# Performance work log

Measured on AMD Instinct MI355X. Metric: run time of the kernel, lower is better.

Reference implementation:

```python
import jax, jax.numpy as jnp
import numpy as np

HIDDEN = 4096
N_HEADS = 32
N_KV = 8
HEAD_DIM = 128
ROPE_THETA = 10000.0
B, S = 2, 2048


def _rope_neox(x, cos, sin):
    # x: [B,S,H,D]; cos/sin: [B,S,1,D/2]
    half = x.shape[-1] // 2
    x1, x2 = x[..., :half], x[..., half:]
    return jnp.concatenate([x1 * cos - x2 * sin, x2 * cos + x1 * sin], axis=-1)


def setup_inputs() -> dict:
    key = jax.random.key(0)
    k1, k2, k3 = jax.random.split(key, 3)
    hidden_states = jax.random.normal(k1, (B, S, HIDDEN), dtype=jnp.float32)
    positions = jnp.arange(B * S, dtype=jnp.int32).reshape(B, S)
    q_size = N_HEADS * HEAD_DIM
    kv_size = N_KV * HEAD_DIM
    w_qkv = jax.random.normal(k2, (HIDDEN, q_size + 2 * kv_size), dtype=jnp.float32) * (HIDDEN ** -0.5)
    w_o = jax.random.normal(k3, (q_size, HIDDEN), dtype=jnp.float32) * (q_size ** -0.5)
    return {"hidden_states": hidden_states, "positions": positions, "w_qkv": w_qkv, "w_o": w_o}


def reference(hidden_states, positions, w_qkv, w_o):
    q_size = N_HEADS * HEAD_DIM
    kv_size = N_KV * HEAD_DIM
    b, s, _ = hidden_states.shape

    qkv = hidden_states @ w_qkv  # [B,S,q+2kv]
    q = qkv[..., :q_size].reshape(b, s, N_HEADS, HEAD_DIM)
    k = qkv[..., q_size:q_size + kv_size].reshape(b, s, N_KV, HEAD_DIM)
    v = qkv[..., q_size + kv_size:].reshape(b, s, N_KV, HEAD_DIM)

    # RoPE (neox style, full rotary dim)
    inv_freq = 1.0 / (ROPE_THETA ** (jnp.arange(0, HEAD_DIM, 2, dtype=jnp.float32) / HEAD_DIM))
    ang = positions.astype(jnp.float32)[..., None] * inv_freq  # [B,S,D/2]
    cos = jnp.cos(ang)[:, :, None, :]
    sin = jnp.sin(ang)[:, :, None, :]
    q = _rope_neox(q, cos, sin)
    k = _rope_neox(k, cos, sin)

    # GQA: expand kv heads to match q heads
    rep = N_HEADS // N_KV
    k = jnp.repeat(k, rep, axis=2)  # [B,S,H,D]
    v = jnp.repeat(v, rep, axis=2)

    scale = HEAD_DIM ** -0.5
    scores = jnp.einsum('bqhd,bkhd->bhqk', q, k) * scale  # [B,H,S,S]
    causal = jnp.tril(jnp.ones((s, s), dtype=bool))
    scores = jnp.where(causal[None, None], scores, jnp.finfo(scores.dtype).min)
    probs = jax.nn.softmax(scores, axis=-1)
    attn = jnp.einsum('bhqk,bkhd->bqhd', probs, v).reshape(b, s, q_size)
    return attn @ w_o
```

## Files before the change

### kernel.cpp

```cpp
#include <hip/hip_runtime.h>
#include <hip/hip_bf16.h>
#include <stdint.h>
#include <stddef.h>

typedef unsigned short u16;
typedef __bf16 bf16x8 __attribute__((ext_vector_type(8)));
typedef float f32x4 __attribute__((ext_vector_type(4)));
typedef float f32x16 __attribute__((ext_vector_type(16)));
typedef unsigned u32x2 __attribute__((ext_vector_type(2)));

#define NH 32
#define NKV 8
#define HD 128
#define QKV_N 6144
#define SEQ 2048

__device__ __forceinline__ u16 f2b(float x) {
  union { float f; unsigned u; } v; v.f = x;
  unsigned r = v.u + 0x7FFF + ((v.u >> 16) & 1);
  return (u16)(r >> 16);
}
__device__ __forceinline__ float b2f(u16 b) {
  union { float f; unsigned u; } v; v.u = ((unsigned)b) << 16;
  return v.f;
}
__device__ __forceinline__ void gload16(const void* g, void* l) {
  __builtin_amdgcn_global_load_lds((const __attribute__((address_space(1))) unsigned int*)g,
                                   (__attribute__((address_space(3))) unsigned int*)l, 16, 0, 0);
}
template <int N>
__device__ __forceinline__ void vmwait() {
  asm volatile("s_waitcnt vmcnt(%0)" ::"n"(N) : "memory");
}
__device__ __forceinline__ unsigned pk(float lo, float hi) {
  union { __bf16 h[2]; unsigned w; } u;
  u.h[0] = (__bf16)lo; u.h[1] = (__bf16)hi;
  return u.w;
}
__device__ __forceinline__ void plswap(unsigned& a, unsigned& b) {
  u32x2 r = __builtin_amdgcn_permlane32_swap(a, b, false, false);
  a = r.x; b = r.y;
}
__device__ __forceinline__ float pl_partner_max(float x) {
  unsigned u = __float_as_uint(x);
  u32x2 r = __builtin_amdgcn_permlane32_swap(u, u, false, false);
  return fmaxf(__uint_as_float(r.x), __uint_as_float(r.y));
}
__device__ __forceinline__ float pl_partner_sum(float x) {
  unsigned u = __float_as_uint(x);
  u32x2 r = __builtin_amdgcn_permlane32_swap(u, u, false, false);
  return __uint_as_float(r.x) + __uint_as_float(r.y);
}

__global__ void cast_f32_bf16(const float* __restrict__ in, u16* __restrict__ out, int n) {
  int i = (blockIdx.x * blockDim.x + threadIdx.x) * 4;
  if (i >= n) return;
  float4 v = *(const float4*)&in[i];
  ushort4 o;
  o.x = f2b(v.x); o.y = f2b(v.y); o.z = f2b(v.z); o.w = f2b(v.w);
  *(ushort4*)&out[i] = o;
}

__global__ void cast_transpose(const float* __restrict__ in, u16* __restrict__ out, int K, int N) {
  __shared__ float t[32][33];
  int n0 = blockIdx.x * 32, k0 = blockIdx.y * 32;
  int tx = threadIdx.x, ty = threadIdx.y;
#pragma unroll
  for (int i = 0; i < 4; ++i)
    t[ty + i * 8][tx] = in[(size_t)(k0 + ty + i * 8) * N + n0 + tx];
  __syncthreads();
#pragma unroll
  for (int i = 0; i < 4; ++i)
    out[(size_t)(n0 + ty + i * 8) * K + k0 + tx] = f2b(t[tx][ty + i * 8]);
}

__device__ __forceinline__ void storeC(float* C, size_t i, float v) { C[i] = v; }
__device__ __forceinline__ void storeC(u16* C, size_t i, float v) { C[i] = f2b(v); }

#define MFMA16(q, A0, A1, B0, B1)                                                              \
  {                                                                                            \
    _Pragma("unroll") for (int mi = 0; mi < 4; ++mi)                                           \
      _Pragma("unroll") for (int ni = 0; ni < 2; ++ni)                                         \
        acc[q][mi][ni] = __builtin_amdgcn_mfma_f32_16x16x32_bf16(A0[mi], B0[ni], acc[q][mi][ni], 0, 0, 0); \
    _Pragma("unroll") for (int mi = 0; mi < 4; ++mi)                                           \
      _Pragma("unroll") for (int ni = 0; ni < 2; ++ni)                                         \
        acc[q][mi][ni] = __builtin_amdgcn_mfma_f32_16x16x32_bf16(A1[mi], B1[ni], acc[q][mi][ni], 0, 0, 0); \
  }

#define KT256(NOFF, SGHI, SGLO, HASV0, HASV1, VM1)                                             \
  {                                                                                            \
    bf16x8 a0[4], a1[4], bl0[2], bl1[2], bh0[2], bh1[2];                                       \
                             \
    _Pragma("unroll") for (int mi = 0; mi < 4; ++mi) {                                         \
      a0[mi] = *(const bf16x8*)(rA0 + (NOFF) + mi * 1024);                                     \
      a1[mi] = *(const bf16x8*)(rA1 + (NOFF) + mi * 1024);                                     \
    }                                                                                          \
    _Pragma("unroll") for (int ni = 0; ni < 2; ++ni) {                                         \
      bl0[ni] = *(const bf16x8*)(rB0 + (NOFF) + ni * 1024);                                    \
      bl1[ni] = *(const bf16x8*)(rB1 + (NOFF) + ni * 1024);                                    \
      bh0[ni] = *(const bf16x8*)(rB0 + (NOFF) + 8192 + ni * 1024);                             \
      bh1[ni] = *(const bf16x8*)(rB1 + (NOFF) + 8192 + ni * 1024);                             \
    }                                                                                          \
    if (SGHI) {                                                                                \
      gload16(pAhi0, dAhi0 + ((NOFF) ^ 16384)); gload16(pAhi1, dAhi1 + ((NOFF) ^ 16384));      \
      pAhi0 += 64; pAhi1 += 64;                                                                \
      gload16(pBlo0, dBlo0 + ((NOFF) ^ 16384)); gload16(pBlo1, dBlo1 + ((NOFF) ^ 16384));      \
      gload16(pBhi0, dBhi0 + ((NOFF) ^ 16384)); gload16(pBhi1, dBhi1 + ((NOFF) ^ 16384));      \
      pBlo0 += 64; pBlo1 += 64; pBhi0 += 64; pBhi1 += 64;                                      \
    }                                                                                          \
    __builtin_amdgcn_s_barrier();                                                              \
    __builtin_amdgcn_s_setprio(1);                                                             \
    MFMA16(0, a0, a1, bl0, bl1)                                                                \
    MFMA16(1, a0, a1, bh0, bh1)                                                                \
    __builtin_amdgcn_s_setprio(0);                                                             \
    __builtin_amdgcn_sched_barrier(0);                                                         \
    if (HASV0) vmwait<8>();                                                                    \
    __builtin_amdgcn_s_barrier();                                                              \
                                                    \
    _Pragma("unroll") for (int mi = 0; mi < 4; ++mi) {                                         \
      a0[mi] = *(const bf16x8*)(rA0 + (NOFF) + 8192 + mi * 1024);                              \
      a1[mi] = *(const bf16x8*)(rA1 + (NOFF) + 8192 + mi * 1024);                              \
    }                                                                                          \
    if (SGLO) {                                                                                \
      gload16(pAlo0, dAlo0 + (NOFF)); gload16(pAlo1, dAlo1 + (NOFF));                          \
      pAlo0 += 64; pAlo1 += 64;                                                                \
    }                                                                                          \
    __builtin_amdgcn_s_barrier();                                                              \
    __builtin_amdgcn_s_setprio(1);                                                             \
    MFMA16(2, a0, a1, bl0, bl1)                                                                \
    MFMA16(3, a0, a1, bh0, bh1)                                                                \
    __builtin_amdgcn_s_setprio(0);                                                             \
    __builtin_amdgcn_sched_barrier(0);                                                         \
    if (HASV1) vmwait<VM1>();                                                                  \
    __builtin_amdgcn_s_barrier();                                                              \
  }

template <typename OutT>
__global__ __launch_bounds__(512, 2) void gemm256(const u16* __restrict__ A, const u16* __restrict__ Bt,
                                                  OutT* __restrict__ C, int M, int N, int K) {
  __shared__ __align__(16) u16 sA[2 * 16384];
  __shared__ __align__(16) u16 sB[2 * 16384];
  const int nbx = N >> 8;
  const int nwg = (M >> 8) * nbx;
  const int cpx = nwg >> 3;
  const int wg = ((int)blockIdx.x & 7) * cpx + ((int)blockIdx.x >> 3);
  const int row0 = (wg / nbx) << 8, col0 = (wg % nbx) << 8;
  const int tid = threadIdx.x, w = tid >> 6, lane = tid & 63;
  const int wm = w >> 2, wn = w & 3;
  const int lq = lane & 15, lh = lane >> 4, x7 = lq & 7;
  const int o0 = (lh ^ x7) << 3, o1 = ((4 + lh) ^ x7) << 3;
  const int nt = K >> 6;

  const int rr = tid >> 3;
  const int swz = ((tid & 7) ^ (rr & 7)) << 3;
  const u16* pAlo0 = A + (size_t)(row0 + rr) * K + swz;
  const u16* pAlo1 = A + (size_t)(row0 + 64 + rr) * K + swz;
  const u16* pAhi0 = A + (size_t)(row0 + 128 + rr) * K + swz;
  const u16* pAhi1 = A + (size_t)(row0 + 192 + rr) * K + swz;
  const u16* pBlo0 = Bt + (size_t)(col0 + rr) * K + swz;
  const u16* pBlo1 = Bt + (size_t)(col0 + 64 + rr) * K + swz;
  const u16* pBhi0 = Bt + (size_t)(col0 + 128 + rr) * K + swz;
  const u16* pBhi1 = Bt + (size_t)(col0 + 192 + rr) * K + swz;
  u16* dAlo0 = sA + w * 512;
  u16* dAlo1 = sA + 4096 + w * 512;
  u16* dAhi0 = sA + 8192 + w * 512;
  u16* dAhi1 = sA + 12288 + w * 512;
  u16* dBlo0 = sB + w * 512;
  u16* dBlo1 = sB + 4096 + w * 512;
  u16* dBhi0 = sB + 8192 + w * 512;
  u16* dBhi1 = sB + 12288 + w * 512;
  const u16* rA0 = sA + (wm * 64 + lq) * 64 + o0;
  const u16* rA1 = sA + (wm * 64 + lq) * 64 + o1;
  const u16* rB0 = sB + (wn * 32 + lq) * 64 + o0;
  const u16* rB1 = sB + (wn * 32 + lq) * 64 + o1;

  f32x4 acc[4][4][2] = {};

  gload16(pAlo0, dAlo0); gload16(pAlo1, dAlo1); pAlo0 += 64; pAlo1 += 64;
  gload16(pBlo0, dBlo0); gload16(pBlo1, dBlo1); pBlo0 += 64; pBlo1 += 64;
  gload16(pBhi0, dBhi0); gload16(pBhi1, dBhi1); pBhi0 += 64; pBhi1 += 64;
  gload16(pAhi0, dAhi0); gload16(pAhi1, dAhi1); pAhi0 += 64; pAhi1 += 64;
  gload16(pAlo0, dAlo0 + 16384); gload16(pAlo1, dAlo1 + 16384); pAlo0 += 64; pAlo1 += 64;
  vmwait<4>();
  __builtin_amdgcn_s_barrier();

  for (int t = 0; t < nt - 2; t += 2) {
    KT256(0, 1, 1, 1, 1, 2)
    KT256(16384, 1, 1, 1, 1, 2)
  }
  KT256(0, 1, 0, 1, 1, 0)
  KT256(16384, 0, 0, 0, 0, 0)

#pragma unroll
  for (int q = 0; q < 4; ++q) {
    const int ah = q >> 1, bh2 = q & 1;
#pragma unroll
    for (int mi = 0; mi < 4; ++mi)
#pragma unroll
      for (int ni = 0; ni < 2; ++ni)
#pragma unroll
        for (int j = 0; j < 4; ++j) {
          const int row = row0 + ah * 128 + wm * 64 + mi * 16 + lh * 4 + j;
          const int col = col0 + bh2 * 128 + wn * 32 + ni * 16 + lq;
          storeC(C, (size_t)row * N + col, acc[q][mi][ni][j]);
        }
  }
}

#define MM24(q, A0, A1)                                                                        \
  {                                                                                            \
    _Pragma("unroll") for (int mi = 0; mi < 4; ++mi)                                           \
      _Pragma("unroll") for (int ni = 0; ni < 3; ++ni)                                         \
        acc[q][mi][ni] = __builtin_amdgcn_mfma_f32_16x16x32_bf16(A0[mi], b0[ni], acc[q][mi][ni], 0, 0, 0); \
    _Pragma("unroll") for (int mi = 0; mi < 4; ++mi)                                           \
      _Pragma("unroll") for (int ni = 0; ni < 3; ++ni)                                         \
        acc[q][mi][ni] = __builtin_amdgcn_mfma_f32_16x16x32_bf16(A1[mi], b1[ni], acc[q][mi][ni], 0, 0, 0); \
  }

#define KT192(NA, NB, SGHI, SGLO, HASV0, HASV1, VM1)                                           \
  {                                                                                            \
    bf16x8 a0[4], a1[4], b0[3], b1[3];                                                         \
    _Pragma("unroll") for (int mi = 0; mi < 4; ++mi) {                                         \
      a0[mi] = *(const bf16x8*)(rA0 + (NA) + mi * 1024);                                       \
      a1[mi] = *(const bf16x8*)(rA1 + (NA) + mi * 1024);                                       \
    }                                                                                          \
    _Pragma("unroll") for (int ni = 0; ni < 3; ++ni) {                                         \
      b0[ni] = *(const bf16x8*)(rB0 + (NB) + ni * 1024);                                       \
      b1[ni] = *(const bf16x8*)(rB1 + (NB) + ni * 1024);                                       \
    }                                                                                          \
    if (SGHI) {                                                                                \
      gload16(pA2, dA2 + ((NA) ^ 16384)); gload16(pA3, dA3 + ((NA) ^ 16384));                  \
      pA2 += 64; pA3 += 64;                                                                    \
      gload16(pB0, dB0 + ((NB) ^ 12288)); gload16(pB1, dB1 + ((NB) ^ 12288));                  \
      gload16(pB2, dB2 + ((NB) ^ 12288));                                                      \
      pB0 += 64; pB1 += 64; pB2 += 64;                                                         \
    }                                                                                          \
    __builtin_amdgcn_s_barrier();                                                              \
    __builtin_amdgcn_s_setprio(1);                                                             \
    MM24(0, a0, a1)                                                                            \
    __builtin_amdgcn_s_setprio(0);                                                             \
    __builtin_amdgcn_sched_barrier(0);                                                         \
    if (HASV0) vmwait<7>();                                                                    \
    __builtin_amdgcn_s_barrier();                                                              \
    _Pragma("unroll") for (int mi = 0; mi < 4; ++mi) {                                         \
      a0[mi] = *(const bf16x8*)(rA0 + (NA) + 8192 + mi * 1024);                                \
      a1[mi] = *(const bf16x8*)(rA1 + (NA) + 8192 + mi * 1024);                                \
    }                                                                                          \
    if (SGLO) {                                                                                \
      gload16(pA0, dA0 + (NA)); gload16(pA1, dA1 + (NA));                                      \
      pA0 += 64; pA1 += 64;                                                                    \
    }                                                                                          \
    __builtin_amdgcn_s_barrier();                                                              \
    __builtin_amdgcn_s_setprio(1);                                                             \
    MM24(1, a0, a1)                                                                            \
    __builtin_amdgcn_s_setprio(0);                                                             \
    __builtin_amdgcn_sched_barrier(0);                                                         \
    if (HASV1) vmwait<VM1>();                                                                  \
    __builtin_amdgcn_s_barrier();                                                              \
  }

__global__ __launch_bounds__(512, 2) void gemm192(const u16* __restrict__ A, const u16* __restrict__ Bt,
                                                  u16* __restrict__ C, int M, int N, int K) {
  __shared__ __align__(16) u16 sA[2 * 16384];
  __shared__ __align__(16) u16 sB[2 * 12288];
  const int nbx = N / 192;
  const int nwg = (M >> 8) * nbx;
  const int cpx = nwg >> 3;
  const int wg = ((int)blockIdx.x & 7) * cpx + ((int)blockIdx.x >> 3);
  const int row0 = (wg / nbx) << 8, col0 = (wg % nbx) * 192;
  const int tid = threadIdx.x, w = tid >> 6, lane = tid & 63;
  const int wm = w >> 2, wn = w & 3;
  const int lq = lane & 15, lh = lane >> 4, x7 = lq & 7;
  const int o0 = (lh ^ x7) << 3, o1 = ((4 + lh) ^ x7) << 3;
  const int nt = K >> 6;

  const int rr = tid >> 3;
  const int swz = ((tid & 7) ^ (rr & 7)) << 3;
  const u16* pA0 = A + (size_t)(row0 + rr) * K + swz;
  const u16* pA1 = A + (size_t)(row0 + 64 + rr) * K + swz;
  const u16* pA2 = A + (size_t)(row0 + 128 + rr) * K + swz;
  const u16* pA3 = A + (size_t)(row0 + 192 + rr) * K + swz;
  const u16* pB0 = Bt + (size_t)(col0 + rr) * K + swz;
  const u16* pB1 = Bt + (size_t)(col0 + 64 + rr) * K + swz;
  const u16* pB2 = Bt + (size_t)(col0 + 128 + rr) * K + swz;
  u16* dA0 = sA + w * 512;
  u16* dA1 = sA + 4096 + w * 512;
  u16* dA2 = sA + 8192 + w * 512;
  u16* dA3 = sA + 12288 + w * 512;
  u16* dB0 = sB + w * 512;
  u16* dB1 = sB + 4096 + w * 512;
  u16* dB2 = sB + 8192 + w * 512;
  const u16* rA0 = sA + (wm * 64 + lq) * 64 + o0;
  const u16* rA1 = sA + (wm * 64 + lq) * 64 + o1;
  const u16* rB0 = sB + (wn * 48 + lq) * 64 + o0;
  const u16* rB1 = sB + (wn * 48 + lq) * 64 + o1;

  f32x4 acc[2][4][3] = {};

  gload16(pA0, dA0); gload16(pA1, dA1); pA0 += 64; pA1 += 64;
  gload16(pB0, dB0); gload16(pB1, dB1); gload16(pB2, dB2); pB0 += 64; pB1 += 64; pB2 += 64;
  gload16(pA2, dA2); gload16(pA3, dA3); pA2 += 64; pA3 += 64;
  gload16(pA0, dA0 + 16384); gload16(pA1, dA1 + 16384); pA0 += 64; pA1 += 64;
  vmwait<4>();
  __builtin_amdgcn_s_barrier();

  for (int t = 0; t < nt - 2; t += 2) {
    KT192(0, 0, 1, 1, 1, 1, 2)
    KT192(16384, 12288, 1, 1, 1, 1, 2)
  }
  KT192(0, 0, 1, 0, 1, 1, 0)
  KT192(16384, 12288, 0, 0, 0, 0, 0)

#pragma unroll
  for (int ah = 0; ah < 2; ++ah)
#pragma unroll
    for (int mi = 0; mi < 4; ++mi)
#pragma unroll
      for (int ni = 0; ni < 3; ++ni)
#pragma unroll
        for (int j = 0; j < 4; ++j) {
          const int row = row0 + ah * 128 + wm * 64 + mi * 16 + lh * 4 + j;
          const int col = col0 + wn * 48 + ni * 16 + lq;
          C[(size_t)row * N + col] = f2b(acc[ah][mi][ni][j]);
        }
}

__global__ void rope_kernel(u16* __restrict__ qkv, const int* __restrict__ pos, float qscale) {
  __shared__ float cs[64], sn[64];
  const int row = blockIdx.x;
  const int tid = threadIdx.x;
  if (tid < 64) {
    float p = (float)pos[row];
    float inv = exp2f(-(float)tid * 0.20762050593046f);
    float a = p * inv;
    cs[tid] = cosf(a);
    sn[tid] = sinf(a);
  }
  __syncthreads();
  const size_t base = (size_t)row * QKV_N;
  for (int i = tid; i < 40 * 64; i += 256) {
    const int h = i >> 6, d = i & 63;
    const size_t o = base + h * 128 + d;
    float x1 = b2f(qkv[o]), x2 = b2f(qkv[o + 64]);
    float c = cs[d], s = sn[d];
    float o1 = x1 * c - x2 * s;
    float o2 = x2 * c + x1 * s;
    if (h < NH) { o1 *= qscale; o2 *= qscale; }
    qkv[o] = f2b(o1);
    qkv[o + 64] = f2b(o2);
  }
}

__global__ void v_transpose(const u16* __restrict__ qkv, u16* __restrict__ vt) {
  __shared__ u16 t[32][33];
  const int b = blockIdx.z >> 3, kvh = blockIdx.z & 7;
  const int s0 = blockIdx.x * 32, d0 = blockIdx.y * 32;
  const int tx = threadIdx.x, ty = threadIdx.y;
#pragma unroll
  for (int i = 0; i < 4; ++i)
    t[ty + i * 8][tx] = qkv[(size_t)(b * SEQ + s0 + ty + i * 8) * QKV_N + 5120 + kvh * 128 + d0 + tx];
  __syncthreads();
#pragma unroll
  for (int i = 0; i < 4; ++i)
    vt[(size_t)((b * NKV + kvh) * HD + d0 + ty + i * 8) * SEQ + s0 + tx] = t[tx][ty + i * 8];
}

__global__ __launch_bounds__(512, 2) void attn_kernel(const u16* __restrict__ qkv, const u16* __restrict__ vt,
                                                      u16* __restrict__ attn) {
  __shared__ __align__(16) u16 sK[2][64 * 128];
  __shared__ __align__(16) u16 sV[2][128 * 64];
  const int b = blockIdx.z, h = blockIdx.y;
  const int qt = (b == 0) ? blockIdx.x : 7 - blockIdx.x;
  const int kvh = h >> 2;
  const int qb = qt * 256;
  const int tid = threadIdx.x, w = tid >> 6, lane = tid & 63;
  const int lq = lane & 31, hi = lane >> 5, x7 = lane & 7;
  const int qw = qb + (w << 5);
  const int qa = qw + lq;
  const int nt = 4 * (qt + 1);

  auto stage = [&](int buf, int kt) {
    const int k0 = kt * 64;
#pragma unroll
    for (int c = 0; c < 2; ++c) {
      const int g = c * 512 + tid;
      const int r = g >> 4, gc = g & 15;
      const int gs = gc ^ (r & 7);
      gload16(qkv + (size_t)(b * SEQ + k0 + r) * QKV_N + 4096 + kvh * 128 + gs * 8,
              &sK[buf][(c * 512 + (w << 6)) * 8]);
    }
#pragma unroll
    for (int c = 0; c < 2; ++c) {
      const int g = c * 512 + tid;
      const int r = g >> 3, gc = g & 7;
      const int gs = gc ^ (r & 7);
      gload16(vt + (size_t)((b * NKV + kvh) * HD + r) * SEQ + k0 + gs * 8,
              &sV[buf][(c * 512 + (w << 6)) * 8]);
    }
  };

  stage(0, 0);
  bf16x8 qf[8];
#pragma unroll
  for (int ks = 0; ks < 8; ++ks)
    qf[ks] = *(const bf16x8*)&qkv[(size_t)(b * SEQ + qw + lq) * QKV_N + h * 128 + ks * 16 + 8 * hi];

  f32x16 o[4] = {};
  float mreg = -1e30f, lreg = 0.f;

  asm volatile("s_waitcnt vmcnt(0)" ::: "memory");
  __builtin_amdgcn_s_barrier();

  for (int kt = 0; kt < nt; ++kt) {
    const int cur = kt & 1;
    const int k0 = kt * 64;
    if (kt + 1 < nt) {
      stage(cur ^ 1, kt + 1);
      asm volatile("s_waitcnt vmcnt(4)" ::: "memory");
    } else {
      asm volatile("s_waitcnt vmcnt(0)" ::: "memory");
    }
    __builtin_amdgcn_s_barrier();

    if (k0 <= qw + 31) {
      const u16* sk = sK[cur];
      f32x16 st0 = {}, st1 = {};
      __builtin_amdgcn_s_setprio(1);
#pragma unroll
      for (int ks = 0; ks < 8; ++ks) {
        const int g = ((2 * ks + hi) ^ x7) * 8;
        bf16x8 kf0 = *(const bf16x8*)&sk[lq * 128 + g];
        bf16x8 kf1 = *(const bf16x8*)&sk[(32 + lq) * 128 + g];
        st0 = __builtin_amdgcn_mfma_f32_32x32x16_bf16(kf0, qf[ks], st0, 0, 0, 0);
        st1 = __builtin_amdgcn_mfma_f32_32x32x16_bf16(kf1, qf[ks], st1, 0, 0, 0);
      }
      __builtin_amdgcn_s_setprio(0);
      if (k0 + 63 > qw) {
#pragma unroll
        for (int r = 0; r < 16; ++r) {
          const int cr = (r & 3) + 8 * (r >> 2) + 4 * hi;
          st0[r] = (k0 + cr <= qa) ? st0[r] : -1e30f;
          st1[r] = (k0 + 32 + cr <= qa) ? st1[r] : -1e30f;
        }
      }
      float a8[8];
#pragma unroll
      for (int r = 0; r < 8; ++r)
        a8[r] = fmaxf(fmaxf(st0[r], st0[r + 8]), fmaxf(st1[r], st1[r + 8]));
#pragma unroll
      for (int s = 4; s; s >>= 1)
#pragma unroll
        for (int r = 0; r < s; ++r) a8[r] = fmaxf(a8[r], a8[r + s]);
      const float pm = pl_partner_max(a8[0]);
      if (!__all(pm <= mreg + 8.f)) {
        const float mn = fmaxf(mreg, pm);
        const float al = exp2f(mreg - mn);
        lreg *= al;
        mreg = mn;
#pragma unroll
        for (int r = 0; r < 16; ++r) {
          const int cr = (r & 3) + 8 * (r >> 2) + 4 * hi;
          const float ar = __shfl(al, cr, 64);
#pragma unroll
          for (int dn = 0; dn < 4; ++dn) o[dn][r] *= ar;
        }
      }
#pragma unroll
      for (int r = 0; r < 16; ++r) {
        st0[r] = exp2f(st0[r] - mreg);
        st1[r] = exp2f(st1[r] - mreg);
      }
      float s8[8];
#pragma unroll
      for (int r = 0; r < 8; ++r)
        s8[r] = (st0[r] + st0[r + 8]) + (st1[r] + st1[r + 8]);
#pragma unroll
      for (int s = 4; s; s >>= 1)
#pragma unroll
        for (int r = 0; r < s; ++r) s8[r] += s8[r + s];
      lreg += pl_partner_sum(s8[0]);
      union U8 { unsigned w[4]; bf16x8 v; };
      U8 pa[4];
#define PACKFRAG(F, P0, P1, P2, P3, P4, P5, P6, P7)                   \
      {                                                               \
        unsigned a0 = pk(P0, P1), a1 = pk(P2, P3);                    \
        unsigned b0 = pk(P4, P5), b1 = pk(P6, P7);                    \
        plswap(a0, b0); plswap(a1, b1);                               \
        pa[F].w[0] = a0; pa[F].w[1] = a1; pa[F].w[2] = b0; pa[F].w[3] = b1; \
      }
      PACKFRAG(0, st0[0], st0[1], st0[2], st0[3], st0[4], st0[5], st0[6], st0[7])
      PACKFRAG(1, st0[8], st0[9], st0[10], st0[11], st0[12], st0[13], st0[14], st0[15])
      PACKFRAG(2, st1[0], st1[1], st1[2], st1[3], st1[4], st1[5], st1[6], st1[7])
      PACKFRAG(3, st1[8], st1[9], st1[10], st1[11], st1[12], st1[13], st1[14], st1[15])
#undef PACKFRAG
      const u16* sv = sV[cur];
      __builtin_amdgcn_s_setprio(1);
#pragma unroll
      for (int dn = 0; dn < 4; ++dn) {
#pragma unroll
        for (int ks = 0; ks < 4; ++ks) {
          bf16x8 vf = *(const bf16x8*)&sv[(dn * 32 + lq) * 64 + (((2 * ks + hi) ^ x7)) * 8];
          o[dn] = __builtin_amdgcn_mfma_f32_32x32x16_bf16(pa[ks].v, vf, o[dn], 0, 0, 0);
        }
      }
      __builtin_amdgcn_s_setprio(0);
    }
    __builtin_amdgcn_s_barrier();
  }

  const float inv = 1.0f / lreg;
#pragma unroll
  for (int r = 0; r < 16; ++r) {
    const int cr = (r & 3) + 8 * (r >> 2) + 4 * hi;
    const float fr = __shfl(inv, cr, 64);
    const size_t row = (size_t)(b * SEQ + qw + cr);
#pragma unroll
    for (int dn = 0; dn < 4; ++dn)
      attn[row * 4096 + h * 128 + dn * 32 + lq] = f2b(o[dn][r] * fr);
  }
}

extern "C" void kernel_launch(void* const* d_in, const int* in_sizes, int n_in,
                              void* d_out, int out_size, void* d_ws, size_t ws_size,
                              hipStream_t stream) {
  const float* hs = (const float*)d_in[0];
  const int* pos = (const int*)d_in[1];
  const float* w_qkv = (const float*)d_in[2];
  const float* w_o = (const float*)d_in[3];
  float* out = (float*)d_out;
  char* ws = (char*)d_ws;

  u16* hid = (u16*)ws;
  u16* attnb = hid;
  u16* wT = (u16*)(ws + 33554432);
  u16* qkv = (u16*)(ws + 83886080);
  u16* vt = (u16*)(ws + 134217728);

  const float qscale = 0.12751744f;

  cast_f32_bf16<<<16384, 256, 0, stream>>>(hs, hid, 4096 * 4096);
  cast_transpose<<<dim3(192, 128), dim3(32, 8), 0, stream>>>(w_qkv, wT, 4096, QKV_N);
  gemm192<<<512, 512, 0, stream>>>(hid, wT, qkv, 4096, QKV_N, 4096);
  rope_kernel<<<4096, 256, 0, stream>>>(qkv, pos, qscale);
  v_transpose<<<dim3(64, 4, 16), dim3(32, 8), 0, stream>>>(qkv, vt);
  cast_transpose<<<dim3(128, 128), dim3(32, 8), 0, stream>>>(w_o, wT, 4096, 4096);
  attn_kernel<<<dim3(8, 32, 2), 512, 0, stream>>>(qkv, vt, attnb);
  gemm256<float><<<256, 512, 0, stream>>>(attnb, wT, out, 4096, 4096, 4096);
}
```

Baseline: 522.3 us.

## Single-buffer A tile in QKV GEMM for higher occupancy; vectorize RoPE

```diff
diff --git a/kernel.cpp b/kernel.cpp
--- a/kernel.cpp
+++ b/kernel.cpp
@@ -90,7 +90,6 @@
 #define KT256(NOFF, SGHI, SGLO, HASV0, HASV1, VM1)                                             \
   {                                                                                            \
     bf16x8 a0[4], a1[4], bl0[2], bl1[2], bh0[2], bh1[2];                                       \
-                             \
     _Pragma("unroll") for (int mi = 0; mi < 4; ++mi) {                                         \
       a0[mi] = *(const bf16x8*)(rA0 + (NOFF) + mi * 1024);                                     \
       a1[mi] = *(const bf16x8*)(rA1 + (NOFF) + mi * 1024);                                     \
@@ -116,7 +115,6 @@
     __builtin_amdgcn_sched_barrier(0);                                                         \
     if (HASV0) vmwait<8>();                                                                    \
     __builtin_amdgcn_s_barrier();                                                              \
-                                                    \
     _Pragma("unroll") for (int mi = 0; mi < 4; ++mi) {                                         \
       a0[mi] = *(const bf16x8*)(rA0 + (NOFF) + 8192 + mi * 1024);                              \
       a1[mi] = *(const bf16x8*)(rA1 + (NOFF) + 8192 + mi * 1024);                              \
@@ -217,20 +215,19 @@
         acc[q][mi][ni] = __builtin_amdgcn_mfma_f32_16x16x32_bf16(A1[mi], b1[ni], acc[q][mi][ni], 0, 0, 0); \
   }
 
-#define KT192(NA, NB, SGHI, SGLO, HASV0, HASV1, VM1)                                           \
+#define KTS(NB, SGB, SGA, VMEND)                                                               \
   {                                                                                            \
     bf16x8 a0[4], a1[4], b0[3], b1[3];                                                         \
+                                                          \
     _Pragma("unroll") for (int mi = 0; mi < 4; ++mi) {                                         \
-      a0[mi] = *(const bf16x8*)(rA0 + (NA) + mi * 1024);                                       \
-      a1[mi] = *(const bf16x8*)(rA1 + (NA) + mi * 1024);                                       \
+      a0[mi] = *(const bf16x8*)(rA0 + mi * 1024);                                              \
+      a1[mi] = *(const bf16x8*)(rA1 + mi * 1024);                                              \
     }                                                                                          \
     _Pragma("unroll") for (int ni = 0; ni < 3; ++ni) {                                         \
       b0[ni] = *(const bf16x8*)(rB0 + (NB) + ni * 1024);                                       \
       b1[ni] = *(const bf16x8*)(rB1 + (NB) + ni * 1024);                                       \
     }                                                                                          \
-    if (SGHI) {                                                                                \
-      gload16(pA2, dA2 + ((NA) ^ 16384)); gload16(pA3, dA3 + ((NA) ^ 16384));                  \
-      pA2 += 64; pA3 += 64;                                                                    \
+    if (SGB) {                                                                                 \
       gload16(pB0, dB0 + ((NB) ^ 12288)); gload16(pB1, dB1 + ((NB) ^ 12288));                  \
       gload16(pB2, dB2 + ((NB) ^ 12288));                                                      \
       pB0 += 64; pB1 += 64; pB2 += 64;                                                         \
@@ -240,28 +237,30 @@
     MM24(0, a0, a1)                                                                            \
     __builtin_amdgcn_s_setprio(0);                                                             \
     __builtin_amdgcn_sched_barrier(0);                                                         \
-    if (HASV0) vmwait<7>();                                                                    \
-    __builtin_amdgcn_s_barrier();                                                              \
+    __builtin_amdgcn_s_barrier();                                                              \
+                                     \
     _Pragma("unroll") for (int mi = 0; mi < 4; ++mi) {                                         \
-      a0[mi] = *(const bf16x8*)(rA0 + (NA) + 8192 + mi * 1024);                                \
-      a1[mi] = *(const bf16x8*)(rA1 + (NA) + 8192 + mi * 1024);                                \
-    }                                                                                          \
-    if (SGLO) {                                                                                \
-      gload16(pA0, dA0 + (NA)); gload16(pA1, dA1 + (NA));                                      \
-      pA0 += 64; pA1 += 64;                                                                    \
-    }                                                                                          \
-    __builtin_amdgcn_s_barrier();                                                              \
+      a0[mi] = *(const bf16x8*)(rA0 + 8192 + mi * 1024);                                       \
+      a1[mi] = *(const bf16x8*)(rA1 + 8192 + mi * 1024);                                       \
+    }                                                                                          \
+    asm volatile("s_waitcnt lgkmcnt(0)" ::: "memory");                                         \
+    __builtin_amdgcn_sched_barrier(0);                                                         \
+    __builtin_amdgcn_s_barrier();                                                              \
+    if (SGA) {                                                                                 \
+      gload16(pA0, dA0); gload16(pA1, dA1); gload16(pA2, dA2); gload16(pA3, dA3);              \
+      pA0 += 64; pA1 += 64; pA2 += 64; pA3 += 64;                                              \
+    }                                                                                          \
     __builtin_amdgcn_s_setprio(1);                                                             \
     MM24(1, a0, a1)                                                                            \
     __builtin_amdgcn_s_setprio(0);                                                             \
     __builtin_amdgcn_sched_barrier(0);                                                         \
-    if (HASV1) vmwait<VM1>();                                                                  \
-    __builtin_amdgcn_s_barrier();                                                              \
-  }
-
-__global__ __launch_bounds__(512, 2) void gemm192(const u16* __restrict__ A, const u16* __restrict__ Bt,
-                                                  u16* __restrict__ C, int M, int N, int K) {
-  __shared__ __align__(16) u16 sA[2 * 16384];
+    if (VMEND) vmwait<0>();                                                                    \
+    __builtin_amdgcn_s_barrier();                                                              \
+  }
+
+__global__ __launch_bounds__(512, 4) void gemm192s(const u16* __restrict__ A, const u16* __restrict__ Bt,
+                                                   u16* __restrict__ C, int M, int N, int K) {
+  __shared__ __align__(16) u16 sA[16384];
   __shared__ __align__(16) u16 sB[2 * 12288];
   const int nbx = N / 192;
   const int nwg = (M >> 8) * nbx;
@@ -297,19 +296,19 @@
 
   f32x4 acc[2][4][3] = {};
 
-  gload16(pA0, dA0); gload16(pA1, dA1); pA0 += 64; pA1 += 64;
-  gload16(pB0, dB0); gload16(pB1, dB1); gload16(pB2, dB2); pB0 += 64; pB1 += 64; pB2 += 64;
-  gload16(pA2, dA2); gload16(pA3, dA3); pA2 += 64; pA3 += 64;
-  gload16(pA0, dA0 + 16384); gload16(pA1, dA1 + 16384); pA0 += 64; pA1 += 64;
-  vmwait<4>();
+  gload16(pA0, dA0); gload16(pA1, dA1); gload16(pA2, dA2); gload16(pA3, dA3);
+  pA0 += 64; pA1 += 64; pA2 += 64; pA3 += 64;
+  gload16(pB0, dB0); gload16(pB1, dB1); gload16(pB2, dB2);
+  pB0 += 64; pB1 += 64; pB2 += 64;
+  vmwait<0>();
   __builtin_amdgcn_s_barrier();
 
   for (int t = 0; t < nt - 2; t += 2) {
-    KT192(0, 0, 1, 1, 1, 1, 2)
-    KT192(16384, 12288, 1, 1, 1, 1, 2)
-  }
-  KT192(0, 0, 1, 0, 1, 1, 0)
-  KT192(16384, 12288, 0, 0, 0, 0, 0)
+    KTS(0, 1, 1, 1)
+    KTS(12288, 1, 1, 1)
+  }
+  KTS(0, 1, 1, 1)
+  KTS(12288, 0, 0, 0)
 
 #pragma unroll
   for (int ah = 0; ah < 2; ++ah)
@@ -338,16 +337,31 @@
   }
   __syncthreads();
   const size_t base = (size_t)row * QKV_N;
-  for (int i = tid; i < 40 * 64; i += 256) {
-    const int h = i >> 6, d = i & 63;
-    const size_t o = base + h * 128 + d;
-    float x1 = b2f(qkv[o]), x2 = b2f(qkv[o + 64]);
-    float c = cs[d], s = sn[d];
-    float o1 = x1 * c - x2 * s;
-    float o2 = x2 * c + x1 * s;
-    if (h < NH) { o1 *= qscale; o2 *= qscale; }
-    qkv[o] = f2b(o1);
-    qkv[o + 64] = f2b(o2);
+  for (int i = tid; i < 40 * 16; i += 256) {
+    const int h = i >> 4, dq = (i & 15) * 4;
+    const size_t o = base + h * 128 + dq;
+    ushort4 v1 = *(const ushort4*)&qkv[o];
+    ushort4 v2 = *(const ushort4*)&qkv[o + 64];
+    const float sc = (h < NH) ? qscale : 1.0f;
+    ushort4 r1, r2;
+    {
+      float x1 = b2f(v1.x), x2 = b2f(v2.x), c = cs[dq], s = sn[dq];
+      r1.x = f2b((x1 * c - x2 * s) * sc); r2.x = f2b((x2 * c + x1 * s) * sc);
+    }
+    {
+      float x1 = b2f(v1.y), x2 = b2f(v2.y), c = cs[dq + 1], s = sn[dq + 1];
+      r1.y = f2b((x1 * c - x2 * s) * sc); r2.y = f2b((x2 * c + x1 * s) * sc);
+    }
+    {
+      float x1 = b2f(v1.z), x2 = b2f(v2.z), c = cs[dq + 2], s = sn[dq + 2];
+      r1.z = f2b((x1 * c - x2 * s) * sc); r2.z = f2b((x2 * c + x1 * s) * sc);
+    }
+    {
+      float x1 = b2f(v1.w), x2 = b2f(v2.w), c = cs[dq + 3], s = sn[dq + 3];
+      r1.w = f2b((x1 * c - x2 * s) * sc); r2.w = f2b((x2 * c + x1 * s) * sc);
+    }
+    *(ushort4*)&qkv[o] = r1;
+    *(ushort4*)&qkv[o + 64] = r2;
   }
 }
 
@@ -540,7 +554,7 @@
 
   cast_f32_bf16<<<16384, 256, 0, stream>>>(hs, hid, 4096 * 4096);
   cast_transpose<<<dim3(192, 128), dim3(32, 8), 0, stream>>>(w_qkv, wT, 4096, QKV_N);
-  gemm192<<<512, 512, 0, stream>>>(hid, wT, qkv, 4096, QKV_N, 4096);
+  gemm192s<<<512, 512, 0, stream>>>(hid, wT, qkv, 4096, QKV_N, 4096);
   rope_kernel<<<4096, 256, 0, stream>>>(qkv, pos, qscale);
   v_transpose<<<dim3(64, 4, 16), dim3(32, 8), 0, stream>>>(qkv, vt);
   cast_transpose<<<dim3(128, 128), dim3(32, 8), 0, stream>>>(w_o, wT, 4096, 4096);
```

After: 1.867 ms. +257.5%, slower.
